# Performance work log

Measured on AMD Instinct MI355X. Metric: run time of the kernel, lower is better.

Reference implementation:

```python
import jax, jax.numpy as jnp
import numpy as np

B, W, F = 64, 128, 64          # batch, window (node feat dim), n_features (nodes)
H, OUTW = 4, 128               # num_heads, out window size
NEG_SLOPE = 0.2                # LeakyReLU negative slope (alpha)


def setup_inputs() -> dict:
    key = jax.random.key(0)
    ks = jax.random.split(key, 6)
    scale_in = 1.0 / np.sqrt(W)
    scale_a = 1.0 / np.sqrt(OUTW)
    return {
        "x": jax.random.normal(ks[0], (B, W, F), dtype=jnp.float32),
        "W_src": jax.random.normal(ks[1], (H * OUTW, W), dtype=jnp.float32) * scale_in,
        "b_src": jnp.zeros((H * OUTW,), dtype=jnp.float32),
        "W_dst": jax.random.normal(ks[2], (H * OUTW, W), dtype=jnp.float32) * scale_in,
        "b_dst": jnp.zeros((H * OUTW,), dtype=jnp.float32),
        "attn": jax.random.normal(ks[3], (H, OUTW), dtype=jnp.float32) * scale_a,
    }


def reference(x, W_src, b_src, W_dst, b_dst, attn):
    # x: [B, W, F] -> node features nf: [B, F, W] (F nodes, W-dim features)
    nf = jnp.transpose(x, (0, 2, 1))
    b, f, w = nf.shape
    h, outw = attn.shape
    # GATv2 separate source/destination projections (share_weights=False)
    fs = (nf @ W_src.T + b_src).reshape(b, f, h, outw)  # [B, F, H, outW]
    fd = (nf @ W_dst.T + b_dst).reshape(b, f, h, outw)
    # additive score over complete graph with self-loops: e[b,i,j,h,d]
    s = fs[:, :, None, :, :] + fd[:, None, :, :, :]      # [B, src, dst, H, outW]
    e = jnp.where(s >= 0, s, NEG_SLOPE * s)              # LeakyReLU
    scores = jnp.einsum('bijhd,hd->bhij', e, attn)       # [B, H, src, dst]
    # edge softmax: normalize over incoming edges (sources) per destination
    a = jax.nn.softmax(scores, axis=2)
    # weighted scatter-sum aggregation at destinations
    out = jnp.einsum('bhij,bihd->bjhd', a, fs)           # [B, F, H, outW]
    out = out.mean(axis=2)                               # mean over heads -> [B, F, outW]
    return jnp.transpose(out, (0, 2, 1))                 # [B, outW, F]
```

## Files before the change

kernel.cpp:

```cpp
#include <hip/hip_runtime.h>
#include <math.h>

#define BB 64
#define WW 128
#define FF 64
#define HH 4
#define OW 128


struct GemmRegion {
    float xq[32 * 64];
    float wq[2 * 128 * 36];
};
struct AttnRegion {
    float fsl[64 * 132];
    float fdl[64 * 132];
    float st[64 * 68];
    float A6[OW], B4[OW];
    float cs[FF], cd[FF];
    float redm[8 * 64];
    float reds[8 * 64];
    float invl[64];
};
union SMem { GemmRegion g; AttnRegion a; };

__global__ __launch_bounds__(512) void gat_fused(
    const float* __restrict__ x,
    const float* __restrict__ Wsrc,
    const float* __restrict__ bsrc,
    const float* __restrict__ Wdst,
    const float* __restrict__ bdst,
    const float* __restrict__ attn,
    float* __restrict__ out)
{
    __shared__ __align__(16) SMem sm;
    __shared__ float bl[2 * 128];

    const int bx = blockIdx.x;
    const int h  = bx & 3;
    const int b  = bx >> 2;
    const int t  = threadIdx.x;

    const int m  = t >> 8;
    const int i0 = (t & 15) * 4;
    const int d0 = ((t >> 4) & 15) * 8;

    if (t < 256) bl[t] = (t & 128 ? bdst : bsrc)[h * 128 + (t & 127)];

    float acc[8][4] = {};

    for (int kq = 0; kq < 4; ++kq) {
        if (kq) __syncthreads();
        {
            const float4* xs = (const float4*)(x + ((size_t)b * WW + kq * 32) * FF);
            ((float4*)sm.g.xq)[t] = xs[t];
        }
        #pragma unroll
        for (int p = 0; p < 4; ++p) {
            int idx = p * 512 + t;
            int mm = idx >> 10, d = (idx >> 3) & 127, q = idx & 7;
            const float* src = (mm ? Wdst : Wsrc)
                             + (size_t)(h * 128 + d) * WW + kq * 32 + q * 4;
            *(float4*)&sm.g.wq[(mm * 128 + d) * 36 + q * 4] = *(const float4*)src;
        }
        __syncthreads();

        #pragma unroll
        for (int k0 = 0; k0 < 32; k0 += 4) {
            float4 xv[4];
            #pragma unroll
            for (int kk = 0; kk < 4; ++kk)
                xv[kk] = *(const float4*)&sm.g.xq[(k0 + kk) * 64 + i0];
            float4 wv[8];
            #pragma unroll
            for (int dd = 0; dd < 8; ++dd)
                wv[dd] = *(const float4*)&sm.g.wq[(m * 128 + d0 + dd) * 36 + k0];
            #pragma unroll
            for (int kk = 0; kk < 4; ++kk) {
                const float* xf = (const float*)&xv[kk];
                #pragma unroll
                for (int dd = 0; dd < 8; ++dd) {
                    const float wf = ((const float*)&wv[dd])[kk];
                    acc[dd][0] = fmaf(xf[0], wf, acc[dd][0]);
                    acc[dd][1] = fmaf(xf[1], wf, acc[dd][1]);
                    acc[dd][2] = fmaf(xf[2], wf, acc[dd][2]);
                    acc[dd][3] = fmaf(xf[3], wf, acc[dd][3]);
                }
            }
        }
    }
    __syncthreads();

    {
        float* dst = m ? sm.a.fdl : sm.a.fsl;
        #pragma unroll
        for (int ii = 0; ii < 4; ++ii) {
            #pragma unroll
            for (int dq = 0; dq < 2; ++dq) {
                float4 o;
                o.x = acc[dq * 4 + 0][ii] + bl[m * 128 + d0 + dq * 4 + 0];
                o.y = acc[dq * 4 + 1][ii] + bl[m * 128 + d0 + dq * 4 + 1];
                o.z = acc[dq * 4 + 2][ii] + bl[m * 128 + d0 + dq * 4 + 2];
                o.w = acc[dq * 4 + 3][ii] + bl[m * 128 + d0 + dq * 4 + 3];
                *(float4*)&dst[(i0 + ii) * 132 + d0 + dq * 4] = o;
            }
        }
        if (t < 128) {
            float av = attn[h * OW + t];
            sm.a.A6[t] = 0.6f * av;
            sm.a.B4[t] = 0.4f * av;
        }
    }
    __syncthreads();

    if (t < 64) {
        float s = 0.0f;
        #pragma unroll 8
        for (int c = 0; c < 32; ++c) {
            float4 fv = *(const float4*)&sm.a.fsl[t * 132 + c * 4];
            float4 av = *(const float4*)&sm.a.A6[c * 4];
            s = fmaf(fv.x, av.x, fmaf(fv.y, av.y, fmaf(fv.z, av.z, fmaf(fv.w, av.w, s))));
        }
        sm.a.cs[t] = s;
    } else if (t < 128) {
        const int j = t - 64;
        float s = 0.0f;
        #pragma unroll 8
        for (int c = 0; c < 32; ++c) {
            float4 fv = *(const float4*)&sm.a.fdl[j * 132 + c * 4];
            float4 av = *(const float4*)&sm.a.A6[c * 4];
            s = fmaf(fv.x, av.x, fmaf(fv.y, av.y, fmaf(fv.z, av.z, fmaf(fv.w, av.w, s))));
        }
        sm.a.cd[j] = s;
    }
    __syncthreads();

    {
        const int lane = t & 63;
        const int jl0  = (t >> 6) * 8;
        float sc[8] = {};
        #pragma unroll 4
        for (int c = 0; c < 32; ++c) {
            const int dd0 = c * 4;
            float4 fsv = *(const float4*)&sm.a.fsl[lane * 132 + dd0];
            float4 b4  = *(const float4*)&sm.a.B4[dd0];
            #pragma unroll
            for (int jj = 0; jj < 8; ++jj) {
                float4 fdv = *(const float4*)&sm.a.fdl[(jl0 + jj) * 132 + dd0];
                float r = sc[jj];
                r = fmaf(b4.x, fabsf(fsv.x + fdv.x), r);
                r = fmaf(b4.y, fabsf(fsv.y + fdv.y), r);
                r = fmaf(b4.z, fabsf(fsv.z + fdv.z), r);
                r = fmaf(b4.w, fabsf(fsv.w + fdv.w), r);
                sc[jj] = r;
            }
        }
        const float csl = sm.a.cs[lane];
        float4 o0, o1;
        o0.x = sc[0] + csl + sm.a.cd[jl0 + 0];
        o0.y = sc[1] + csl + sm.a.cd[jl0 + 1];
        o0.z = sc[2] + csl + sm.a.cd[jl0 + 2];
        o0.w = sc[3] + csl + sm.a.cd[jl0 + 3];
        o1.x = sc[4] + csl + sm.a.cd[jl0 + 4];
        o1.y = sc[5] + csl + sm.a.cd[jl0 + 5];
        o1.z = sc[6] + csl + sm.a.cd[jl0 + 6];
        o1.w = sc[7] + csl + sm.a.cd[jl0 + 7];
        *(float4*)&sm.a.st[lane * 68 + jl0]     = o0;
        *(float4*)&sm.a.st[lane * 68 + jl0 + 4] = o1;
    }
    __syncthreads();

    {
        const int j = t & 63, st8 = t >> 6;
        const int i0s = st8 * 8;
        float mx = sm.a.st[i0s * 68 + j];
        #pragma unroll
        for (int k = 1; k < 8; ++k) mx = fmaxf(mx, sm.a.st[(i0s + k) * 68 + j]);
        sm.a.redm[st8 * 64 + j] = mx;
    }
    __syncthreads();
    {
        const int j = t & 63, st8 = t >> 6;
        const int i0s = st8 * 8;
        float mj = sm.a.redm[j];
        #pragma unroll
        for (int s2 = 1; s2 < 8; ++s2) mj = fmaxf(mj, sm.a.redm[s2 * 64 + j]);
        float ps = 0.0f;
        #pragma unroll
        for (int k = 0; k < 8; ++k) {
            float e = __expf(sm.a.st[(i0s + k) * 68 + j] - mj);
            sm.a.st[(i0s + k) * 68 + j] = e;
            ps += e;
        }
        sm.a.reds[st8 * 64 + j] = ps;
    }
    __syncthreads();
    if (t < 64) {
        float l = 0.0f;
        #pragma unroll
        for (int s2 = 0; s2 < 8; ++s2) l += sm.a.reds[s2 * 64 + t];
        sm.a.invl[t] = 0.25f / l;
    }
    __syncthreads();

    {
        const int j = t & 63, dblk = t >> 6;
        float ag[16] = {};
        #pragma unroll 4
        for (int i = 0; i < FF; ++i) {
            const float p = sm.a.st[i * 68 + j];
            const float* fr = &sm.a.fsl[i * 132 + dblk * 16];
            float4 f0 = *(const float4*)(fr);
            float4 f1 = *(const float4*)(fr + 4);
            float4 f2 = *(const float4*)(fr + 8);
            float4 f3 = *(const float4*)(fr + 12);
            ag[0]  = fmaf(p, f0.x, ag[0]);  ag[1]  = fmaf(p, f0.y, ag[1]);
            ag[2]  = fmaf(p, f0.z, ag[2]);  ag[3]  = fmaf(p, f0.w, ag[3]);
            ag[4]  = fmaf(p, f1.x, ag[4]);  ag[5]  = fmaf(p, f1.y, ag[5]);
            ag[6]  = fmaf(p, f1.z, ag[6]);  ag[7]  = fmaf(p, f1.w, ag[7]);
            ag[8]  = fmaf(p, f2.x, ag[8]);  ag[9]  = fmaf(p, f2.y, ag[9]);
            ag[10] = fmaf(p, f2.z, ag[10]); ag[11] = fmaf(p, f2.w, ag[11]);
            ag[12] = fmaf(p, f3.x, ag[12]); ag[13] = fmaf(p, f3.y, ag[13]);
            ag[14] = fmaf(p, f3.z, ag[14]); ag[15] = fmaf(p, f3.w, ag[15]);
        }
        const float iv = sm.a.invl[j];
        float* ob = out + ((size_t)b * OW + dblk * 16) * FF + j;
        #pragma unroll
        for (int e = 0; e < 16; ++e)
            atomicAdd(ob + e * FF, ag[e] * iv);
    }
}

extern "C" void kernel_launch(void* const* d_in, const int* in_sizes, int n_in,
                              void* d_out, int out_size, void* d_ws, size_t ws_size,
                              hipStream_t stream) {
    const float* x    = (const float*)d_in[0];
    const float* Wsrc = (const float*)d_in[1];
    const float* bsrc = (const float*)d_in[2];
    const float* Wdst = (const float*)d_in[3];
    const float* bdst = (const float*)d_in[4];
    const float* attn = (const float*)d_in[5];

    hipMemsetAsync(d_out, 0, (size_t)out_size, stream);
    gat_fused<<<BB * HH, 512, 0, stream>>>(x, Wsrc, bsrc, Wdst, bdst, attn,
                                           (float*)d_out);
}
```

Measured before the change: 106.6 us.

## Double block size to 1024 threads and rebalance per-thread work across phases

Launches 1024 threads per block instead of 512 and halves each thread's work in every phase: projection GEMM tiles (4x4 instead of 8x4, K staged in 64-wide chunks), score rows, softmax reduction slices, and aggregation columns. The linear score terms are split across 256 threads and reduced when summed, and one barrier is removed by folding the inverse-sum computation into the aggregation phase. The goal is more in-flight wavefronts to hide LDS latency with only 256 blocks in the grid. The trade-off is more barrier cost per block, a larger shared-memory GEMM staging area, and fewer registers for reuse.

```diff
diff --git a/kernel.cpp b/kernel.cpp
--- a/kernel.cpp
+++ b/kernel.cpp
@@ -9,22 +9,20 @@
 
 
 struct GemmRegion {
-    float xq[32 * 64];
-    float wq[2 * 128 * 36];
+    float xq[64 * 64];
+    float wq[2 * 128 * 68];
 };
 struct AttnRegion {
-    float fsl[64 * 132];
-    float fdl[64 * 132];
-    float st[64 * 68];
+    float fsl[FF * 132];
+    float fdl[FF * 132];
+    float st[FF * 68];
     float A6[OW], B4[OW];
-    float cs[FF], cd[FF];
-    float redm[8 * 64];
-    float reds[8 * 64];
-    float invl[64];
+    float redm[16 * 64];
+    float reds[16 * 64];
 };
 union SMem { GemmRegion g; AttnRegion a; };
 
-__global__ __launch_bounds__(512) void gat_fused(
+__global__ __launch_bounds__(1024) void gat_fused(
     const float* __restrict__ x,
     const float* __restrict__ Wsrc,
     const float* __restrict__ bsrc,
@@ -41,50 +39,51 @@
     const int b  = bx >> 2;
     const int t  = threadIdx.x;
 
-    const int m  = t >> 8;
+    const int m  = t >> 9;
     const int i0 = (t & 15) * 4;
-    const int d0 = ((t >> 4) & 15) * 8;
+    const int g2 = (t >> 4) & 31;
+    const int d0 = (g2 >> 2) * 16 + (g2 & 3) * 4;
 
     if (t < 256) bl[t] = (t & 128 ? bdst : bsrc)[h * 128 + (t & 127)];
 
-    float acc[8][4] = {};
-
-    for (int kq = 0; kq < 4; ++kq) {
-        if (kq) __syncthreads();
+    float acc[4][4] = {};
+
+    for (int kh = 0; kh < 2; ++kh) {
+        if (kh) __syncthreads();
         {
-            const float4* xs = (const float4*)(x + ((size_t)b * WW + kq * 32) * FF);
-            ((float4*)sm.g.xq)[t] = xs[t];
+            const int k = t >> 4, iq = t & 15;
+            *(float4*)&sm.g.xq[k * 64 + iq * 4] =
+                *(const float4*)(x + ((size_t)b * WW + kh * 64 + k) * FF + iq * 4);
         }
         #pragma unroll
         for (int p = 0; p < 4; ++p) {
-            int idx = p * 512 + t;
-            int mm = idx >> 10, d = (idx >> 3) & 127, q = idx & 7;
-            const float* src = (mm ? Wdst : Wsrc)
-                             + (size_t)(h * 128 + d) * WW + kq * 32 + q * 4;
-            *(float4*)&sm.g.wq[(mm * 128 + d) * 36 + q * 4] = *(const float4*)src;
+            const int idx = p * 1024 + t;
+            const int mm = idx >> 11, d = (idx >> 4) & 127, q = idx & 15;
+            *(float4*)&sm.g.wq[(mm * 128 + d) * 68 + q * 4] =
+                *(const float4*)((mm ? Wdst : Wsrc)
+                                 + (size_t)(h * 128 + d) * WW + kh * 64 + q * 4);
         }
         __syncthreads();
 
-        #pragma unroll
-        for (int k0 = 0; k0 < 32; k0 += 4) {
-            float4 xv[4];
+        #pragma unroll 4
+        for (int k0 = 0; k0 < 64; k0 += 4) {
+            float4 xv[4], wv[4];
             #pragma unroll
             for (int kk = 0; kk < 4; ++kk)
                 xv[kk] = *(const float4*)&sm.g.xq[(k0 + kk) * 64 + i0];
-            float4 wv[8];
-            #pragma unroll
-            for (int dd = 0; dd < 8; ++dd)
-                wv[dd] = *(const float4*)&sm.g.wq[(m * 128 + d0 + dd) * 36 + k0];
+            #pragma unroll
+            for (int e = 0; e < 4; ++e)
+                wv[e] = *(const float4*)&sm.g.wq[(m * 128 + d0 + e) * 68 + k0];
             #pragma unroll
             for (int kk = 0; kk < 4; ++kk) {
-                const float* xf = (const float*)&xv[kk];
                 #pragma unroll
-                for (int dd = 0; dd < 8; ++dd) {
-                    const float wf = ((const float*)&wv[dd])[kk];
-                    acc[dd][0] = fmaf(xf[0], wf, acc[dd][0]);
-                    acc[dd][1] = fmaf(xf[1], wf, acc[dd][1]);
-                    acc[dd][2] = fmaf(xf[2], wf, acc[dd][2]);
-                    acc[dd][3] = fmaf(xf[3], wf, acc[dd][3]);
+                for (int e = 0; e < 4; ++e) {
+                    const float wf = ((const float*)&wv[e])[kk];
+                    const float* xf = (const float*)&xv[kk];
+                    acc[e][0] = fmaf(xf[0], wf, acc[e][0]);
+                    acc[e][1] = fmaf(xf[1], wf, acc[e][1]);
+                    acc[e][2] = fmaf(xf[2], wf, acc[e][2]);
+                    acc[e][3] = fmaf(xf[3], wf, acc[e][3]);
                 }
             }
         }
@@ -93,59 +92,53 @@
 
     {
         float* dst = m ? sm.a.fdl : sm.a.fsl;
+        const float b0 = bl[m * 128 + d0 + 0];
+        const float b1 = bl[m * 128 + d0 + 1];
+        const float b2 = bl[m * 128 + d0 + 2];
+        const float b3 = bl[m * 128 + d0 + 3];
         #pragma unroll
         for (int ii = 0; ii < 4; ++ii) {
-            #pragma unroll
-            for (int dq = 0; dq < 2; ++dq) {
-                float4 o;
-                o.x = acc[dq * 4 + 0][ii] + bl[m * 128 + d0 + dq * 4 + 0];
-                o.y = acc[dq * 4 + 1][ii] + bl[m * 128 + d0 + dq * 4 + 1];
-                o.z = acc[dq * 4 + 2][ii] + bl[m * 128 + d0 + dq * 4 + 2];
-                o.w = acc[dq * 4 + 3][ii] + bl[m * 128 + d0 + dq * 4 + 3];
-                *(float4*)&dst[(i0 + ii) * 132 + d0 + dq * 4] = o;
-            }
+            float4 o;
+            o.x = acc[0][ii] + b0;
+            o.y = acc[1][ii] + b1;
+            o.z = acc[2][ii] + b2;
+            o.w = acc[3][ii] + b3;
+            *(float4*)&dst[(i0 + ii) * 132 + d0] = o;
         }
         if (t < 128) {
-            float av = attn[h * OW + t];
+            const float av = attn[h * OW + t];
             sm.a.A6[t] = 0.6f * av;
             sm.a.B4[t] = 0.4f * av;
         }
     }
     __syncthreads();
 
-    if (t < 64) {
+    if (t < 256) {
+        const int i = t & 63, sel = t >> 6;
+        const float* src = (sel < 2 ? sm.a.fsl : sm.a.fdl) + i * 132 + (sel & 1) * 64;
+        const float* a6  = sm.a.A6 + (sel & 1) * 64;
         float s = 0.0f;
+        #pragma unroll
+        for (int c = 0; c < 16; ++c) {
+            float4 fv = *(const float4*)&src[c * 4];
+            float4 av = *(const float4*)&a6[c * 4];
+            s = fmaf(fv.x, av.x, fmaf(fv.y, av.y, fmaf(fv.z, av.z, fmaf(fv.w, av.w, s))));
+        }
+        sm.a.redm[sel * 64 + i] = s;
+    }
+    __syncthreads();
+
+    {
+        const int lane = t & 63;
+        const int jl0  = (t >> 6) * 4;
+        float sc[4] = {};
         #pragma unroll 8
-        for (int c = 0; c < 32; ++c) {
-            float4 fv = *(const float4*)&sm.a.fsl[t * 132 + c * 4];
-            float4 av = *(const float4*)&sm.a.A6[c * 4];
-            s = fmaf(fv.x, av.x, fmaf(fv.y, av.y, fmaf(fv.z, av.z, fmaf(fv.w, av.w, s))));
-        }
-        sm.a.cs[t] = s;
-    } else if (t < 128) {
-        const int j = t - 64;
-        float s = 0.0f;
-        #pragma unroll 8
-        for (int c = 0; c < 32; ++c) {
-            float4 fv = *(const float4*)&sm.a.fdl[j * 132 + c * 4];
-            float4 av = *(const float4*)&sm.a.A6[c * 4];
-            s = fmaf(fv.x, av.x, fmaf(fv.y, av.y, fmaf(fv.z, av.z, fmaf(fv.w, av.w, s))));
-        }
-        sm.a.cd[j] = s;
-    }
-    __syncthreads();
-
-    {
-        const int lane = t & 63;
-        const int jl0  = (t >> 6) * 8;
-        float sc[8] = {};
-        #pragma unroll 4
         for (int c = 0; c < 32; ++c) {
             const int dd0 = c * 4;
             float4 fsv = *(const float4*)&sm.a.fsl[lane * 132 + dd0];
             float4 b4  = *(const float4*)&sm.a.B4[dd0];
             #pragma unroll
-            for (int jj = 0; jj < 8; ++jj) {
+            for (int jj = 0; jj < 4; ++jj) {
                 float4 fdv = *(const float4*)&sm.a.fdl[(jl0 + jj) * 132 + dd0];
                 float r = sc[jj];
                 r = fmaf(b4.x, fabsf(fsv.x + fdv.x), r);
@@ -155,78 +148,64 @@
                 sc[jj] = r;
             }
         }
-        const float csl = sm.a.cs[lane];
-        float4 o0, o1;
-        o0.x = sc[0] + csl + sm.a.cd[jl0 + 0];
-        o0.y = sc[1] + csl + sm.a.cd[jl0 + 1];
-        o0.z = sc[2] + csl + sm.a.cd[jl0 + 2];
-        o0.w = sc[3] + csl + sm.a.cd[jl0 + 3];
-        o1.x = sc[4] + csl + sm.a.cd[jl0 + 4];
-        o1.y = sc[5] + csl + sm.a.cd[jl0 + 5];
-        o1.z = sc[6] + csl + sm.a.cd[jl0 + 6];
-        o1.w = sc[7] + csl + sm.a.cd[jl0 + 7];
-        *(float4*)&sm.a.st[lane * 68 + jl0]     = o0;
-        *(float4*)&sm.a.st[lane * 68 + jl0 + 4] = o1;
-    }
-    __syncthreads();
-
-    {
-        const int j = t & 63, st8 = t >> 6;
-        const int i0s = st8 * 8;
+        const float csl = sm.a.redm[lane] + sm.a.redm[64 + lane];
+        float4 o;
+        o.x = sc[0] + csl + sm.a.redm[128 + jl0 + 0] + sm.a.redm[192 + jl0 + 0];
+        o.y = sc[1] + csl + sm.a.redm[128 + jl0 + 1] + sm.a.redm[192 + jl0 + 1];
+        o.z = sc[2] + csl + sm.a.redm[128 + jl0 + 2] + sm.a.redm[192 + jl0 + 2];
+        o.w = sc[3] + csl + sm.a.redm[128 + jl0 + 3] + sm.a.redm[192 + jl0 + 3];
+        *(float4*)&sm.a.st[lane * 68 + jl0] = o;
+    }
+    __syncthreads();
+
+    {
+        const int j = t & 63, s = t >> 6;
+        const int i0s = s * 4;
         float mx = sm.a.st[i0s * 68 + j];
         #pragma unroll
-        for (int k = 1; k < 8; ++k) mx = fmaxf(mx, sm.a.st[(i0s + k) * 68 + j]);
-        sm.a.redm[st8 * 64 + j] = mx;
-    }
-    __syncthreads();
-    {
-        const int j = t & 63, st8 = t >> 6;
-        const int i0s = st8 * 8;
+        for (int k = 1; k < 4; ++k) mx = fmaxf(mx, sm.a.st[(i0s + k) * 68 + j]);
+        sm.a.redm[s * 64 + j] = mx;
+    }
+    __syncthreads();
+    {
+        const int j = t & 63, s = t >> 6;
+        const int i0s = s * 4;
         float mj = sm.a.redm[j];
         #pragma unroll
-        for (int s2 = 1; s2 < 8; ++s2) mj = fmaxf(mj, sm.a.redm[s2 * 64 + j]);
+        for (int s2 = 1; s2 < 16; ++s2) mj = fmaxf(mj, sm.a.redm[s2 * 64 + j]);
         float ps = 0.0f;
         #pragma unroll
-        for (int k = 0; k < 8; ++k) {
+        for (int k = 0; k < 4; ++k) {
             float e = __expf(sm.a.st[(i0s + k) * 68 + j] - mj);
             sm.a.st[(i0s + k) * 68 + j] = e;
             ps += e;
         }
-        sm.a.reds[st8 * 64 + j] = ps;
-    }
-    __syncthreads();
-    if (t < 64) {
+        sm.a.reds[s * 64 + j] = ps;
+    }
+    __syncthreads();
+
+    {
+        const int j = t & 63, dblk = t >> 6;
         float l = 0.0f;
         #pragma unroll
-        for (int s2 = 0; s2 < 8; ++s2) l += sm.a.reds[s2 * 64 + t];
-        sm.a.invl[t] = 0.25f / l;
-    }
-    __syncthreads();
-
-    {
-        const int j = t & 63, dblk = t >> 6;
-        float ag[16] = {};
+        for (int s2 = 0; s2 < 16; ++s2) l += sm.a.reds[s2 * 64 + j];
+        const float iv = 0.25f / l;
+
+        float ag[8] = {};
         #pragma unroll 4
         for (int i = 0; i < FF; ++i) {
             const float p = sm.a.st[i * 68 + j];
-            const float* fr = &sm.a.fsl[i * 132 + dblk * 16];
+            const float* fr = &sm.a.fsl[i * 132 + dblk * 8];
             float4 f0 = *(const float4*)(fr);
             float4 f1 = *(const float4*)(fr + 4);
-            float4 f2 = *(const float4*)(fr + 8);
-            float4 f3 = *(const float4*)(fr + 12);
-            ag[0]  = fmaf(p, f0.x, ag[0]);  ag[1]  = fmaf(p, f0.y, ag[1]);
-            ag[2]  = fmaf(p, f0.z, ag[2]);  ag[3]  = fmaf(p, f0.w, ag[3]);
-            ag[4]  = fmaf(p, f1.x, ag[4]);  ag[5]  = fmaf(p, f1.y, ag[5]);
-            ag[6]  = fmaf(p, f1.z, ag[6]);  ag[7]  = fmaf(p, f1.w, ag[7]);
-            ag[8]  = fmaf(p, f2.x, ag[8]);  ag[9]  = fmaf(p, f2.y, ag[9]);
-            ag[10] = fmaf(p, f2.z, ag[10]); ag[11] = fmaf(p, f2.w, ag[11]);
-            ag[12] = fmaf(p, f3.x, ag[12]); ag[13] = fmaf(p, f3.y, ag[13]);
-            ag[14] = fmaf(p, f3.z, ag[14]); ag[15] = fmaf(p, f3.w, ag[15]);
-        }
-        const float iv = sm.a.invl[j];
-        float* ob = out + ((size_t)b * OW + dblk * 16) * FF + j;
-        #pragma unroll
-        for (int e = 0; e < 16; ++e)
+            ag[0] = fmaf(p, f0.x, ag[0]);  ag[1] = fmaf(p, f0.y, ag[1]);
+            ag[2] = fmaf(p, f0.z, ag[2]);  ag[3] = fmaf(p, f0.w, ag[3]);
+            ag[4] = fmaf(p, f1.x, ag[4]);  ag[5] = fmaf(p, f1.y, ag[5]);
+            ag[6] = fmaf(p, f1.z, ag[6]);  ag[7] = fmaf(p, f1.w, ag[7]);
+        }
+        float* ob = out + ((size_t)b * OW + dblk * 8) * FF + j;
+        #pragma unroll
+        for (int e = 0; e < 8; ++e)
             atomicAdd(ob + e * FF, ag[e] * iv);
     }
 }
@@ -242,6 +221,6 @@
     const float* attn = (const float*)d_in[5];
 
     hipMemsetAsync(d_out, 0, (size_t)out_size, stream);
-    gat_fused<<<BB * HH, 512, 0, stream>>>(x, Wsrc, bsrc, Wdst, bdst, attn,
-                                           (float*)d_out);
+    gat_fused<<<BB * HH, 1024, 0, stream>>>(x, Wsrc, bsrc, Wdst, bdst, attn,
+                                            (float*)d_out);
 }
```

New measurement: 105.1 us. Within noise of the previous version (-1.3%).
